# Kernel optimization log

Measured on AMD Instinct MI355X. Metric: run time of the kernel, lower is better.

The kernel has to match this reference:

```python
import jax, jax.numpy as jnp
import numpy as np

B, N, DIM, C_IN, C_OUT = 2, 512, 3, 64, 64


def setup_inputs() -> dict:
    key = jax.random.key(0)
    ks = jax.random.split(key, 9)
    geom = jax.random.normal(ks[0], (B, N, DIM, C_IN), dtype=jnp.float32)
    adj = jax.random.uniform(ks[1], (B, N, N, 1, 1), dtype=jnp.float32)
    rel = jax.random.normal(ks[2], (B, N, N, DIM, 1), dtype=jnp.float32)
    emb = jax.random.normal(ks[3], (B, N, N, 1), dtype=jnp.float32)
    # learned parameters
    theta = jax.random.normal(ks[4], (C_IN + 1, C_OUT), dtype=jnp.float32) * 0.1
    norm_w = jax.random.normal(ks[5], (C_IN + 1, 1), dtype=jnp.float32) * 0.1
    norm_b = jax.random.normal(ks[6], (1,), dtype=jnp.float32) * 0.1
    alpha = jax.random.normal(ks[7], (1, 1, C_OUT), dtype=jnp.float32) * 0.1
    beta = jax.random.normal(ks[8], (1, 1, C_OUT), dtype=jnp.float32) * 0.1
    return {
        "geometric_information": geom,
        "adjacency_matrix": adj,
        "relative_point_cloud": rel,
        "embed_pc_and_features": emb,
        "theta": theta,
        "norm_w": norm_w,
        "norm_b": norm_b,
        "alpha": alpha,
        "beta": beta,
    }


def reference(geometric_information, adjacency_matrix, relative_point_cloud,
              embed_pc_and_features, theta, norm_w, norm_b, alpha, beta):
    b, n, d, c_in = geometric_information.shape
    # broadcast sender features to all pairs: [B,n,n,3,C_in]
    g2 = jnp.broadcast_to(geometric_information[:, None], (b, n, n, d, c_in))
    # concat relative coords as an extra channel: [B,n,n,3,C_in+1]
    embed_x_and_g = jnp.concatenate([g2, relative_point_cloud], axis=-1)
    # use_all_norms branch (block_id != 0): per-channel L2 norm over spatial axis
    norms = jnp.sqrt(jnp.sum(embed_x_and_g * embed_x_and_g, axis=-2))  # [B,n,n,C_in+1]
    norm_and_feature = norms @ norm_w + norm_b + embed_pc_and_features  # [B,n,n,1]
    # P_alpha_beta: affine + activation -> [B,n,n,C_out]
    p_alpha_beta = jax.nn.relu(alpha * norm_and_feature + beta)
    # channel mixing: [B,n,n,3,C_out]
    mixed = embed_x_and_g @ theta
    # adjacency-masked sum over neighbor axis -> [B,n,3,C_out]
    out = jnp.sum(mixed * p_alpha_beta[..., None, :] * adjacency_matrix, axis=2)
    return out
```

## Files before the change

kernel.cpp:

```cpp
#include <hip/hip_runtime.h>
#include <math.h>

#define NPT 512
#define NBJ (2 * NPT)

__global__ __launch_bounds__(64) void precompute_kernel(
    const float* __restrict__ geom,
    const float* __restrict__ theta,
    const float* __restrict__ norm_w,
    const float* __restrict__ norm_b,
    float* __restrict__ s,
    float* __restrict__ gm)
{
    const int bj  = blockIdx.x;
    const int tid = threadIdx.x;
    __shared__ float g[192];

    const float* gb = geom + (size_t)bj * 192;
    g[tid]       = gb[tid];
    g[tid + 64]  = gb[tid + 64];
    g[tid + 128] = gb[tid + 128];
    __syncthreads();

    {
        float g0 = g[tid], g1 = g[64 + tid], g2 = g[128 + tid];
        float t = sqrtf(g0 * g0 + g1 * g1 + g2 * g2) * norm_w[tid];
        for (int off = 32; off > 0; off >>= 1) t += __shfl_down(t, off);
        if (tid == 0) s[bj] = t + norm_b[0];
    }

    float a0 = 0.f, a1 = 0.f, a2 = 0.f;
    for (int c = 0; c < 64; ++c) {
        float th = theta[c * 64 + tid];
        a0 = fmaf(g[c],       th, a0);
        a1 = fmaf(g[64 + c],  th, a1);
        a2 = fmaf(g[128 + c], th, a2);
    }
    float* gmb = gm + (size_t)bj * 192;
    gmb[tid]       = a0;
    gmb[64 + tid]  = a1;
    gmb[128 + tid] = a2;
}

__global__ __launch_bounds__(256) void main_kernel(
    const float* __restrict__ adj,
    const float* __restrict__ rel,
    const float* __restrict__ emb,
    const float* __restrict__ theta,
    const float* __restrict__ norm_w,
    const float* __restrict__ alpha,
    const float* __restrict__ beta,
    const float* __restrict__ s,
    const float* __restrict__ gm,
    float* __restrict__ out)
{
    const int bi   = blockIdx.x;
    const int b    = bi >> 9;
    const int tid  = threadIdx.x;
    const int lane = tid & 63;
    const int wv   = tid >> 6;

    __shared__ float rel_l[1536];
    __shared__ float adj_l[512];
    __shared__ float naf_l[512];

    const float* relb = rel + (size_t)bi * 1536;
    const float* adjb = adj + (size_t)bi * 512;
    const float* embb = emb + (size_t)bi * 512;

    for (int k = tid; k < 1536; k += 256) rel_l[k] = relb[k];
    for (int k = tid; k < 512; k += 256) {
        adj_l[k] = adjb[k];
        naf_l[k] = embb[k];
    }
    __syncthreads();

    const float nw64 = norm_w[64];
    for (int j = tid; j < 512; j += 256) {
        float r0 = rel_l[j * 3], r1 = rel_l[j * 3 + 1], r2 = rel_l[j * 3 + 2];
        naf_l[j] += s[b * 512 + j] + nw64 * sqrtf(r0 * r0 + r1 * r1 + r2 * r2);
    }
    __syncthreads();

    const float al  = alpha[lane];
    const float be  = beta[lane];
    const float t64 = theta[64 * 64 + lane];

    float acc0 = 0.f, acc1 = 0.f, acc2 = 0.f;
    const float* gmb = gm + (size_t)b * (NPT * 192) + lane;
    const int j0 = wv * 128;
    for (int j = j0; j < j0 + 128; ++j) {
        float naf = naf_l[j];
        float p   = fmaxf(fmaf(al, naf, be), 0.f);
        float wvv = adj_l[j] * p;
        const float* gmj = gmb + j * 192;
        float r0 = rel_l[j * 3], r1 = rel_l[j * 3 + 1], r2 = rel_l[j * 3 + 2];
        acc0 = fmaf(wvv, fmaf(r0, t64, gmj[0]),   acc0);
        acc1 = fmaf(wvv, fmaf(r1, t64, gmj[64]),  acc1);
        acc2 = fmaf(wvv, fmaf(r2, t64, gmj[128]), acc2);
    }
    __syncthreads();

    float* red = rel_l;
    red[wv * 192 + lane]       = acc0;
    red[wv * 192 + 64 + lane]  = acc1;
    red[wv * 192 + 128 + lane] = acc2;
    __syncthreads();
    if (tid < 192) {
        float v = red[tid] + red[192 + tid] + red[384 + tid] + red[576 + tid];
        out[(size_t)bi * 192 + tid] = v;
    }
}

extern "C" void kernel_launch(void* const* d_in, const int* in_sizes, int n_in,
                              void* d_out, int out_size, void* d_ws, size_t ws_size,
                              hipStream_t stream) {
    const float* geom   = (const float*)d_in[0];
    const float* adj    = (const float*)d_in[1];
    const float* rel    = (const float*)d_in[2];
    const float* emb    = (const float*)d_in[3];
    const float* theta  = (const float*)d_in[4];
    const float* norm_w = (const float*)d_in[5];
    const float* norm_b = (const float*)d_in[6];
    const float* alpha  = (const float*)d_in[7];
    const float* beta   = (const float*)d_in[8];
    float* out = (float*)d_out;

    float* s  = (float*)d_ws;
    float* gm = s + 1024;

    precompute_kernel<<<NBJ, 64, 0, stream>>>(geom, theta, norm_w, norm_b, s, gm);
    main_kernel<<<NBJ, 256, 0, stream>>>(adj, rel, emb, theta, norm_w, alpha, beta,
                                         s, gm, out);
}
```

Measured before the change: 25.58 us.

## Tile main kernel over i-rows and j-quarters with LDS-staged gm reuse and split reduction

Restructures the pipeline into four kernels. A naf kernel precomputes adjacency-scaled norm features. The main kernel then processes 4 receiver rows per block over one quarter of the neighbours. It streams float4-padded gm tiles into double-buffered LDS through global_load_lds, so the four waves share each gm tile instead of each block re-reading gm from global memory. Partial sums go to workspace and a separate reduce kernel adds them. This trades extra launches and a round trip of intermediates through global memory for better reuse of gm and more overlap of loads with compute.

```diff
diff --git a/kernel.cpp b/kernel.cpp
--- a/kernel.cpp
+++ b/kernel.cpp
@@ -1,8 +1,13 @@
 #include <hip/hip_runtime.h>
 #include <math.h>
 
-#define NPT 512
-#define NBJ (2 * NPT)
+#define WS_S    0
+#define WS_GM4  1024
+#define WS_AN   (1024 + 262144)
+#define WS_PART (1024 + 262144 + 524288)
+
+typedef const __attribute__((address_space(1))) void g_void;
+typedef __attribute__((address_space(3))) void l_void;
 
 __global__ __launch_bounds__(64) void precompute_kernel(
     const float* __restrict__ geom,
@@ -10,7 +15,7 @@
     const float* __restrict__ norm_w,
     const float* __restrict__ norm_b,
     float* __restrict__ s,
-    float* __restrict__ gm)
+    float* __restrict__ gm4)
 {
     const int bj  = blockIdx.x;
     const int tid = threadIdx.x;
@@ -36,80 +41,116 @@
         a1 = fmaf(g[64 + c],  th, a1);
         a2 = fmaf(g[128 + c], th, a2);
     }
-    float* gmb = gm + (size_t)bj * 192;
-    gmb[tid]       = a0;
-    gmb[64 + tid]  = a1;
-    gmb[128 + tid] = a2;
+    float4 v = make_float4(a0, a1, a2, 0.f);
+    *reinterpret_cast<float4*>(gm4 + (size_t)bj * 256 + tid * 4) = v;
+}
+
+__global__ __launch_bounds__(256) void naf_kernel(
+    const float* __restrict__ adj,
+    const float* __restrict__ rel,
+    const float* __restrict__ emb,
+    const float* __restrict__ norm_w,
+    const float* __restrict__ s,
+    float* __restrict__ an)
+{
+    const int bi  = blockIdx.x;
+    const int b   = bi >> 9;
+    const float nw64 = norm_w[64];
+    #pragma unroll
+    for (int k = 0; k < 2; ++k) {
+        int j = threadIdx.x + k * 256;
+        size_t p = (size_t)bi * 512 + j;
+        float r0 = rel[p * 3], r1 = rel[p * 3 + 1], r2 = rel[p * 3 + 2];
+        float naf = s[b * 512 + j] + nw64 * sqrtf(r0 * r0 + r1 * r1 + r2 * r2)
+                  + emb[p];
+        an[p] = adj[p] * naf;
+    }
 }
 
 __global__ __launch_bounds__(256) void main_kernel(
     const float* __restrict__ adj,
     const float* __restrict__ rel,
-    const float* __restrict__ emb,
+    const float* __restrict__ an,
     const float* __restrict__ theta,
-    const float* __restrict__ norm_w,
     const float* __restrict__ alpha,
     const float* __restrict__ beta,
-    const float* __restrict__ s,
-    const float* __restrict__ gm,
-    float* __restrict__ out)
+    const float* __restrict__ gm4,
+    float* __restrict__ part)
 {
-    const int bi   = blockIdx.x;
-    const int b    = bi >> 9;
+    const int bx   = blockIdx.x;
+    const int jq   = bx & 3;
+    const int itg  = bx >> 2;
+    const int b    = itg >> 7;
+    const int i0   = (itg & 127) * 4;
     const int tid  = threadIdx.x;
     const int lane = tid & 63;
     const int wv   = tid >> 6;
+    const int bi   = __builtin_amdgcn_readfirstlane(b * 512 + i0 + wv);
+    const int j0   = jq * 128;
 
-    __shared__ float rel_l[1536];
-    __shared__ float adj_l[512];
-    __shared__ float naf_l[512];
-
-    const float* relb = rel + (size_t)bi * 1536;
-    const float* adjb = adj + (size_t)bi * 512;
-    const float* embb = emb + (size_t)bi * 512;
-
-    for (int k = tid; k < 1536; k += 256) rel_l[k] = relb[k];
-    for (int k = tid; k < 512; k += 256) {
-        adj_l[k] = adjb[k];
-        naf_l[k] = embb[k];
-    }
-    __syncthreads();
-
-    const float nw64 = norm_w[64];
-    for (int j = tid; j < 512; j += 256) {
-        float r0 = rel_l[j * 3], r1 = rel_l[j * 3 + 1], r2 = rel_l[j * 3 + 2];
-        naf_l[j] += s[b * 512 + j] + nw64 * sqrtf(r0 * r0 + r1 * r1 + r2 * r2);
-    }
-    __syncthreads();
+    __shared__ float buf[2][4096];
 
     const float al  = alpha[lane];
     const float be  = beta[lane];
     const float t64 = theta[64 * 64 + lane];
 
+    const float* gmb  = gm4 + ((size_t)b * 512 + j0) * 256;
+    const float* anr  = an  + (size_t)bi * 512 + j0;
+    const float* adjr = adj + (size_t)bi * 512 + j0;
+    const float* relr = rel + ((size_t)bi * 512 + j0) * 3;
+
+    #pragma unroll
+    for (int u = 0; u < 4; ++u) {
+        int unit = u * 4 + wv;
+        __builtin_amdgcn_global_load_lds(
+            (g_void*)(gmb + unit * 256 + lane * 4),
+            (l_void*)(&buf[0][unit * 256]), 16, 0, 0);
+    }
+
     float acc0 = 0.f, acc1 = 0.f, acc2 = 0.f;
-    const float* gmb = gm + (size_t)b * (NPT * 192) + lane;
-    const int j0 = wv * 128;
-    for (int j = j0; j < j0 + 128; ++j) {
-        float naf = naf_l[j];
-        float p   = fmaxf(fmaf(al, naf, be), 0.f);
-        float wvv = adj_l[j] * p;
-        const float* gmj = gmb + j * 192;
-        float r0 = rel_l[j * 3], r1 = rel_l[j * 3 + 1], r2 = rel_l[j * 3 + 2];
-        acc0 = fmaf(wvv, fmaf(r0, t64, gmj[0]),   acc0);
-        acc1 = fmaf(wvv, fmaf(r1, t64, gmj[64]),  acc1);
-        acc2 = fmaf(wvv, fmaf(r2, t64, gmj[128]), acc2);
+    for (int c = 0; c < 8; ++c) {
+        __syncthreads();
+        if (c < 7) {
+            const float* src = gmb + (c + 1) * 4096;
+            #pragma unroll
+            for (int u = 0; u < 4; ++u) {
+                int unit = u * 4 + wv;
+                __builtin_amdgcn_global_load_lds(
+                    (g_void*)(src + unit * 256 + lane * 4),
+                    (l_void*)(&buf[(c + 1) & 1][unit * 256]), 16, 0, 0);
+            }
+        }
+        const float* bp = buf[c & 1];
+        const int jb = c * 16;
+        #pragma unroll 4
+        for (int jj = 0; jj < 16; ++jj) {
+            int j = jb + jj;
+            float s_an  = anr[j];
+            float s_adj = adjr[j];
+            float r0 = relr[j * 3], r1 = relr[j * 3 + 1], r2 = relr[j * 3 + 2];
+            float w = fmaxf(fmaf(al, s_an, be * s_adj), 0.f);
+            float4 g = *reinterpret_cast<const float4*>(bp + (jj << 8) + lane * 4);
+            float t0 = fmaf(r0, t64, g.x);
+            float t1 = fmaf(r1, t64, g.y);
+            float t2 = fmaf(r2, t64, g.z);
+            acc0 = fmaf(w, t0, acc0);
+            acc1 = fmaf(w, t1, acc1);
+            acc2 = fmaf(w, t2, acc2);
+        }
     }
-    __syncthreads();
 
-    float* red = rel_l;
-    red[wv * 192 + lane]       = acc0;
-    red[wv * 192 + 64 + lane]  = acc1;
-    red[wv * 192 + 128 + lane] = acc2;
-    __syncthreads();
-    if (tid < 192) {
-        float v = red[tid] + red[192 + tid] + red[384 + tid] + red[576 + tid];
-        out[(size_t)bi * 192 + tid] = v;
-    }
+    float* pw = part + ((size_t)jq * 1024 + bi) * 192 + lane;
+    pw[0]   = acc0;
+    pw[64]  = acc1;
+    pw[128] = acc2;
+}
+
+__global__ __launch_bounds__(256) void reduce_kernel(
+    const float* __restrict__ part, float* __restrict__ out)
+{
+    int idx = blockIdx.x * 256 + threadIdx.x;
+    out[idx] = part[idx] + part[196608 + idx] + part[2 * 196608 + idx]
+             + part[3 * 196608 + idx];
 }
 
 extern "C" void kernel_launch(void* const* d_in, const int* in_sizes, int n_in,
@@ -126,10 +167,14 @@
     const float* beta   = (const float*)d_in[8];
     float* out = (float*)d_out;
 
-    float* s  = (float*)d_ws;
-    float* gm = s + 1024;
+    float* ws   = (float*)d_ws;
+    float* s    = ws + WS_S;
+    float* gm4  = ws + WS_GM4;
+    float* an   = ws + WS_AN;
+    float* part = ws + WS_PART;
 
-    precompute_kernel<<<NBJ, 64, 0, stream>>>(geom, theta, norm_w, norm_b, s, gm);
-    main_kernel<<<NBJ, 256, 0, stream>>>(adj, rel, emb, theta, norm_w, alpha, beta,
-                                         s, gm, out);
+    precompute_kernel<<<1024, 64, 0, stream>>>(geom, theta, norm_w, norm_b, s, gm4);
+    naf_kernel<<<1024, 256, 0, stream>>>(adj, rel, emb, norm_w, s, an);
+    main_kernel<<<1024, 256, 0, stream>>>(adj, rel, an, theta, alpha, beta, gm4, part);
+    reduce_kernel<<<768, 256, 0, stream>>>(part, out);
 }
```

Result: slower. 38.02 us (+48.7%).

## Split naf computation into separate kernel and tile main kernel over four rows

Applied to the files above, without the earlier changes.

Adds a kernel that computes adj*naf and adj per pair into a packed float2 buffer. The main kernel now handles four output rows per block over half the neighbours, so each float4 load of the padded gm4 row is reused across four rows. Partial sums are combined with atomicAdd after a memset. This aims to cut redundant gm traffic, at the cost of an extra launch, an extra memset, a pk2 round trip through global memory, and non-deterministic atomic summation.

```diff
diff --git a/kernel.cpp b/kernel.cpp
--- a/kernel.cpp
+++ b/kernel.cpp
@@ -1,8 +1,9 @@
 #include <hip/hip_runtime.h>
 #include <math.h>
 
-#define NPT 512
-#define NBJ (2 * NPT)
+#define WS_S   0
+#define WS_GM4 1024
+#define WS_PK2 (1024 + 262144)
 
 __global__ __launch_bounds__(64) void precompute_kernel(
     const float* __restrict__ geom,
@@ -10,7 +11,7 @@
     const float* __restrict__ norm_w,
     const float* __restrict__ norm_b,
     float* __restrict__ s,
-    float* __restrict__ gm)
+    float* __restrict__ gm4)
 {
     const int bj  = blockIdx.x;
     const int tid = threadIdx.x;
@@ -36,79 +37,92 @@
         a1 = fmaf(g[64 + c],  th, a1);
         a2 = fmaf(g[128 + c], th, a2);
     }
-    float* gmb = gm + (size_t)bj * 192;
-    gmb[tid]       = a0;
-    gmb[64 + tid]  = a1;
-    gmb[128 + tid] = a2;
+    *reinterpret_cast<float4*>(gm4 + (size_t)bj * 256 + tid * 4) =
+        make_float4(a0, a1, a2, 0.f);
+}
+
+__global__ __launch_bounds__(256) void naf_kernel(
+    const float* __restrict__ adj,
+    const float* __restrict__ rel,
+    const float* __restrict__ emb,
+    const float* __restrict__ norm_w,
+    const float* __restrict__ s,
+    float* __restrict__ pk2)
+{
+    const int bi = blockIdx.x;
+    const int b  = bi >> 9;
+    const float nw64 = norm_w[64];
+    #pragma unroll
+    for (int k = 0; k < 2; ++k) {
+        int j = threadIdx.x + k * 256;
+        size_t p = (size_t)bi * 512 + j;
+        float r0 = rel[p * 3], r1 = rel[p * 3 + 1], r2 = rel[p * 3 + 2];
+        float naf = s[b * 512 + j] + nw64 * sqrtf(r0 * r0 + r1 * r1 + r2 * r2)
+                  + emb[p];
+        float a = adj[p];
+        *reinterpret_cast<float2*>(pk2 + p * 2) = make_float2(a * naf, a);
+    }
 }
 
 __global__ __launch_bounds__(256) void main_kernel(
-    const float* __restrict__ adj,
     const float* __restrict__ rel,
-    const float* __restrict__ emb,
+    const float* __restrict__ pk2,
     const float* __restrict__ theta,
-    const float* __restrict__ norm_w,
     const float* __restrict__ alpha,
     const float* __restrict__ beta,
-    const float* __restrict__ s,
-    const float* __restrict__ gm,
+    const float* __restrict__ gm4,
     float* __restrict__ out)
 {
-    const int bi   = blockIdx.x;
-    const int b    = bi >> 9;
+    const int bx   = blockIdx.x;
+    const int jh   = bx & 1;
+    const int iq   = (bx >> 1) & 127;
+    const int b    = bx >> 8;
     const int tid  = threadIdx.x;
     const int lane = tid & 63;
-    const int wv   = tid >> 6;
-
-    __shared__ float rel_l[1536];
-    __shared__ float adj_l[512];
-    __shared__ float naf_l[512];
-
-    const float* relb = rel + (size_t)bi * 1536;
-    const float* adjb = adj + (size_t)bi * 512;
-    const float* embb = emb + (size_t)bi * 512;
-
-    for (int k = tid; k < 1536; k += 256) rel_l[k] = relb[k];
-    for (int k = tid; k < 512; k += 256) {
-        adj_l[k] = adjb[k];
-        naf_l[k] = embb[k];
-    }
-    __syncthreads();
-
-    const float nw64 = norm_w[64];
-    for (int j = tid; j < 512; j += 256) {
-        float r0 = rel_l[j * 3], r1 = rel_l[j * 3 + 1], r2 = rel_l[j * 3 + 2];
-        naf_l[j] += s[b * 512 + j] + nw64 * sqrtf(r0 * r0 + r1 * r1 + r2 * r2);
-    }
-    __syncthreads();
+    const int wv   = __builtin_amdgcn_readfirstlane(tid >> 6);
+    const int j0   = jh * 256 + wv * 64;
+    const int bi0  = b * 512 + iq * 4;
 
     const float al  = alpha[lane];
     const float be  = beta[lane];
     const float t64 = theta[64 * 64 + lane];
 
-    float acc0 = 0.f, acc1 = 0.f, acc2 = 0.f;
-    const float* gmb = gm + (size_t)b * (NPT * 192) + lane;
-    const int j0 = wv * 128;
-    for (int j = j0; j < j0 + 128; ++j) {
-        float naf = naf_l[j];
-        float p   = fmaxf(fmaf(al, naf, be), 0.f);
-        float wvv = adj_l[j] * p;
-        const float* gmj = gmb + j * 192;
-        float r0 = rel_l[j * 3], r1 = rel_l[j * 3 + 1], r2 = rel_l[j * 3 + 2];
-        acc0 = fmaf(wvv, fmaf(r0, t64, gmj[0]),   acc0);
-        acc1 = fmaf(wvv, fmaf(r1, t64, gmj[64]),  acc1);
-        acc2 = fmaf(wvv, fmaf(r2, t64, gmj[128]), acc2);
+    const float* gmb = gm4 + ((size_t)(b * 512 + j0)) * 256 + lane * 4;
+
+    float acc[4][3];
+    #pragma unroll
+    for (int il = 0; il < 4; ++il)
+        acc[il][0] = acc[il][1] = acc[il][2] = 0.f;
+
+    #pragma unroll 4
+    for (int jj = 0; jj < 64; ++jj) {
+        float4 g = *reinterpret_cast<const float4*>(gmb + jj * 256);
+        #pragma unroll
+        for (int il = 0; il < 4; ++il) {
+            size_t p = (size_t)(bi0 + il) * 512 + (j0 + jj);
+            float an   = pk2[p * 2];
+            float adjv = pk2[p * 2 + 1];
+            float r0 = rel[p * 3], r1 = rel[p * 3 + 1], r2 = rel[p * 3 + 2];
+            float w = fmaxf(fmaf(al, an, be * adjv), 0.f);
+            acc[il][0] = fmaf(w, fmaf(r0, t64, g.x), acc[il][0]);
+            acc[il][1] = fmaf(w, fmaf(r1, t64, g.y), acc[il][1]);
+            acc[il][2] = fmaf(w, fmaf(r2, t64, g.z), acc[il][2]);
+        }
+    }
+
+    __shared__ float red[4][768];
+    #pragma unroll
+    for (int il = 0; il < 4; ++il) {
+        red[wv][il * 192 + lane]       = acc[il][0];
+        red[wv][il * 192 + 64 + lane]  = acc[il][1];
+        red[wv][il * 192 + 128 + lane] = acc[il][2];
     }
     __syncthreads();
 
-    float* red = rel_l;
-    red[wv * 192 + lane]       = acc0;
-    red[wv * 192 + 64 + lane]  = acc1;
-    red[wv * 192 + 128 + lane] = acc2;
-    __syncthreads();
-    if (tid < 192) {
-        float v = red[tid] + red[192 + tid] + red[384 + tid] + red[576 + tid];
-        out[(size_t)bi * 192 + tid] = v;
+    for (int k = tid; k < 768; k += 256) {
+        float v = red[0][k] + red[1][k] + red[2][k] + red[3][k];
+        int il = k / 192, r = k - il * 192;
+        atomicAdd(&out[(size_t)(bi0 + il) * 192 + r], v);
     }
 }
 
@@ -126,10 +140,13 @@
     const float* beta   = (const float*)d_in[8];
     float* out = (float*)d_out;
 
-    float* s  = (float*)d_ws;
-    float* gm = s + 1024;
+    float* ws  = (float*)d_ws;
+    float* s   = ws + WS_S;
+    float* gm4 = ws + WS_GM4;
+    float* pk2 = ws + WS_PK2;
 
-    precompute_kernel<<<NBJ, 64, 0, stream>>>(geom, theta, norm_w, norm_b, s, gm);
-    main_kernel<<<NBJ, 256, 0, stream>>>(adj, rel, emb, theta, norm_w, alpha, beta,
-                                         s, gm, out);
+    hipMemsetAsync(out, 0, (size_t)out_size * sizeof(float), stream);
+    precompute_kernel<<<1024, 64, 0, stream>>>(geom, theta, norm_w, norm_b, s, gm4);
+    naf_kernel<<<1024, 256, 0, stream>>>(adj, rel, emb, norm_w, s, pk2);
+    main_kernel<<<512, 256, 0, stream>>>(rel, pk2, theta, alpha, beta, gm4, out);
 }
```

Result: slower. 35.45 us (+38.6%).
